# Optimization experiments

Hardware: AMD Instinct MI355X
Metric: run time of the kernel (lower is better)

The kernel has to match this reference:

```python
import jax, jax.numpy as jnp
import numpy as np

N = 65536      # num drones/nodes
E = 262144     # num directed edges
HID = 128      # hidden_dim
HEADS = 8      # gat1 heads
EPS = 1e-5


def _bn(x, g, b):
    # BatchNorm1d in training mode: batch statistics over dim 0 (biased var)
    mu = x.mean(0)
    var = ((x - mu) ** 2).mean(0)
    return (x - mu) * jax.lax.rsqrt(var + EPS) * g + b


def _gat(x, src, dst, W, a_src, a_dst, bias, heads, out_c, n, concat):
    # PyG GATConv math (self-loops already included in src/dst)
    xw = (x @ W).reshape(n, heads, out_c)               # [N,H,C]
    al_s = (xw * a_src).sum(-1)                          # [N,H]
    al_d = (xw * a_dst).sum(-1)                          # [N,H]
    e = jax.nn.leaky_relu(al_s[src] + al_d[dst], 0.2)    # [E',H]
    m = jax.ops.segment_max(e, dst, num_segments=n)      # stable softmax per target
    ex = jnp.exp(e - m[dst])
    den = jax.ops.segment_sum(ex, dst, num_segments=n)
    alpha = ex / den[dst]                                # [E',H]
    out = jax.ops.segment_sum(xw[src] * alpha[:, :, None], dst, num_segments=n)
    out = out.reshape(n, heads * out_c) if concat else out.mean(axis=1)
    return out + bias


def setup_inputs() -> dict:
    key = jax.random.key(0)
    ks = jax.random.split(key, 24)
    s = 0.05
    inp = {
        'node_features': jax.random.normal(ks[0], (N, HID), jnp.float32),
        'relative_poses': jax.random.normal(ks[1], (E, 6), jnp.float32),
        'pe_w1': jax.random.normal(ks[2], (6, 64), jnp.float32) * s,
        'pe_b1': jnp.zeros((64,), jnp.float32),
        'pe_g1': jnp.ones((64,), jnp.float32),
        'pe_be1': jnp.zeros((64,), jnp.float32),
        'pe_w2': jax.random.normal(ks[3], (64, HID), jnp.float32) * s,
        'pe_b2': jnp.zeros((HID,), jnp.float32),
        'pe_g2': jnp.ones((HID,), jnp.float32),
        'pe_be2': jnp.zeros((HID,), jnp.float32),
        'gamma_w': jax.random.normal(ks[4], (HID, HID), jnp.float32) * s,
        'gamma_b': jnp.zeros((HID,), jnp.float32),
        'beta_w': jax.random.normal(ks[5], (HID, HID), jnp.float32) * s,
        'beta_b': jnp.zeros((HID,), jnp.float32),
        'g1_w': jax.random.normal(ks[6], (HID, HEADS * HID), jnp.float32) * s,
        'g1_as': jax.random.normal(ks[7], (HEADS, HID), jnp.float32) * s,
        'g1_ad': jax.random.normal(ks[8], (HEADS, HID), jnp.float32) * s,
        'g1_b': jnp.zeros((HEADS * HID,), jnp.float32),
        'g2_w': jax.random.normal(ks[9], (HEADS * HID, HID), jnp.float32) * s,
        'g2_as': jax.random.normal(ks[10], (1, HID), jnp.float32) * s,
        'g2_ad': jax.random.normal(ks[11], (1, HID), jnp.float32) * s,
        'g2_b': jnp.zeros((HID,), jnp.float32),
        'edge_index': jax.random.randint(ks[12], (2, E), 0, N, jnp.int32),
    }
    return inp


def reference(node_features, relative_poses, pe_w1, pe_b1, pe_g1, pe_be1,
              pe_w2, pe_b2, pe_g2, pe_be2, gamma_w, gamma_b, beta_w, beta_b,
              g1_w, g1_as, g1_ad, g1_b, g2_w, g2_as, g2_ad, g2_b, edge_index):
    src, dst = edge_index[0], edge_index[1]
    # SpatialEncoding: pose MLP with training-mode BN, then FiLM modulation
    h = jax.nn.relu(_bn(relative_poses @ pe_w1 + pe_b1, pe_g1, pe_be1))
    h = jax.nn.relu(_bn(h @ pe_w2 + pe_b2, pe_g2, pe_be2))
    gamma = jax.nn.sigmoid(h @ gamma_w + gamma_b) * 2.0   # [E,HID]
    beta = h @ beta_w + beta_b
    modulated = gamma * node_features[src] + beta          # [E,HID]
    last = jnp.full((N,), -1, jnp.int32).at[dst].max(jnp.arange(E, dtype=jnp.int32))
    enc = jnp.where((last >= 0)[:, None], modulated[jnp.clip(last, 0)], node_features)
    # add self loops (PyG GATConv default)
    loops = jnp.arange(N, dtype=src.dtype)
    src_a = jnp.concatenate([src, loops])
    dst_a = jnp.concatenate([dst, loops])
    x = jax.nn.elu(_gat(enc, src_a, dst_a, g1_w, g1_as, g1_ad, g1_b, HEADS, HID, N, True))
    # dropout is identity in eval mode
    out = _gat(x, src_a, dst_a, g2_w, g2_as, g2_ad, g2_b, 1, HID, N, False)
    return out
```

## Files before the change

### kernel.cpp

```cpp
#include <hip/hip_runtime.h>
#include <hip/hip_bf16.h>
#include <math.h>

#define NN 65536
#define EE 262144

typedef unsigned short u16;
typedef unsigned int u32;
typedef __attribute__((ext_vector_type(8))) short bf16x8;
typedef __attribute__((ext_vector_type(4))) float f32x4;

__device__ __forceinline__ float bfu2f(u16 u){ return __uint_as_float(((u32)u)<<16); }
__device__ __forceinline__ u16 f2bfu(float f){
  u32 x = __float_as_uint(f);
  return (u16)((x + 0x7fffu + ((x>>16)&1u)) >> 16);
}
__device__ __forceinline__ float lrelu(float x){ return x>0.f ? x : 0.2f*x; }
__device__ __forceinline__ float fexp(float x){ return __expf(x); }

__global__ void k_cvtT(const float* __restrict__ B, u16* __restrict__ Bt, int K, int N){
  int idx = blockIdx.x*256+threadIdx.x;
  if (idx < K*N){ int k = idx/N, n = idx - k*N; Bt[n*K+k] = f2bfu(B[idx]); }
}

__global__ void k_cvtn(const float* __restrict__ nf, u16* __restrict__ nfb){
  int i = (blockIdx.x*256+threadIdx.x)*4;
  float4 v = *(const float4*)(nf + i);
  ushort4 o; o.x=f2bfu(v.x); o.y=f2bfu(v.y); o.z=f2bfu(v.z); o.w=f2bfu(v.w);
  *(ushort4*)(nfb + i) = o;
}

__global__ void k_bn1_stats(const float* __restrict__ poses, const float* __restrict__ w1,
                            const float* __restrict__ b1, float* __restrict__ sum1, float* __restrict__ sq1){
  int wave = (blockIdx.x*blockDim.x + threadIdx.x)>>6;
  int c = threadIdx.x & 63;
  float wc[6];
#pragma unroll
  for (int j=0;j<6;++j) wc[j] = w1[j*64+c];
  float bb = b1[c];
  float s=0.f,q=0.f;
  int e0 = wave*(EE/1024);
  for (int e=e0;e<e0+(EE/1024);++e){
    float z = bb;
#pragma unroll
    for (int j=0;j<6;++j) z = fmaf(poses[e*6+j], wc[j], z);
    s += z; q += z*z;
  }
  unsafeAtomicAdd(&sum1[c], s);
  unsafeAtomicAdd(&sq1[c], q);
}

__global__ void k_bn_fin(const float* __restrict__ sum, const float* __restrict__ sq,
                         const float* __restrict__ g, const float* __restrict__ be,
                         const float* __restrict__ bias0,
                         float* __restrict__ a, float* __restrict__ cc, int cols){
  int c = threadIdx.x;
  if (c<cols){
    float mu = sum[c]*(1.f/EE);
    float var = sq[c]*(1.f/EE) - mu*mu;
    float istd = rsqrtf(var + 1e-5f);
    float ac = istd*g[c];
    a[c] = ac;
    float cv = be[c] - mu*ac;
    if (bias0) cv += bias0[c]*ac;
    cc[c] = cv;
  }
}

__global__ void k_red2(const float* __restrict__ psum, const float* __restrict__ psq,
                       float* __restrict__ part2){
  int t = threadIdx.x;
  int b0 = blockIdx.x*128;
  float s = 0.f;
  if (t < 128){
    for (int k=0;k<128;++k) s += psum[(size_t)(b0+k)*128 + t];
  } else {
    int c = t-128;
    for (int k=0;k<128;++k) s += psq[(size_t)(b0+k)*128 + c];
  }
  part2[blockIdx.x*256 + t] = s;
}

__global__ void k_bn_fin2(const float* __restrict__ part2,
                          const float* __restrict__ g, const float* __restrict__ be,
                          const float* __restrict__ bias0,
                          float* __restrict__ a, float* __restrict__ cc){
  int c = threadIdx.x;
  if (c<128){
    float s=0.f,q=0.f;
    for (int k=0;k<32;++k){ s += part2[k*256+c]; q += part2[k*256+128+c]; }
    float mu = s*(1.f/EE);
    float var = q*(1.f/EE) - mu*mu;
    float istd = rsqrtf(var + 1e-5f);
    float ac = istd*g[c];
    a[c] = ac;
    cc[c] = be[c] - mu*ac + bias0[c]*ac;
  }
}

__global__ void k_h1(const float* __restrict__ poses, const float* __restrict__ w1, const float* __restrict__ b1,
                     const float* __restrict__ a1, const float* __restrict__ c1, u16* __restrict__ h1){
  int idx = blockIdx.x*256+threadIdx.x;
  int e = idx>>6, c = idx&63;
  float z = b1[c];
#pragma unroll
  for (int j=0;j<6;++j) z = fmaf(poses[e*6+j], w1[j*64+c], z);
  float h = z*a1[c]+c1[c];
  h1[idx] = f2bfu(h>0.f?h:0.f);
}

template<int EPI>
__launch_bounds__(256)
__global__ void k_mm(const u16* __restrict__ A, const u16* __restrict__ Bt,
                     const u16* __restrict__ Bt2,
                     int K, int lda, int ldbt, int ldc,
                     u16* __restrict__ outb,
                     const float* __restrict__ bias, const float* __restrict__ bias2,
                     float* __restrict__ ssum, float* __restrict__ ssq,
                     const float* __restrict__ gb,
                     const float* __restrict__ bb, const u16* __restrict__ nfselb,
                     const int* __restrict__ lastE){
  const int m0 = blockIdx.x*64, n0 = blockIdx.y*128;
  const int t = threadIdx.x;
  const int lane = t & 63, wv = t>>6;
  const int wr = wv>>1, wc = wv&1;
  __shared__ u16 Als[64*64];
  __shared__ u16 Bls[128*64];
  __shared__ u16 B2ls[EPI==7 ? 128*64 : 8];
  __shared__ float epiS[128][2];
  __shared__ float epiD[128][2];
  f32x4 acc[2][4];
  f32x4 acc2[2][4];
#pragma unroll
  for (int i=0;i<2;++i)
#pragma unroll
    for (int j=0;j<4;++j){ acc[i][j] = (f32x4){0.f,0.f,0.f,0.f}; acc2[i][j] = (f32x4){0.f,0.f,0.f,0.f}; }

  for (int k0=0;k0<K;k0+=64){
    constexpr int NS = (EPI==7) ? 10 : 6;
#pragma unroll
    for (int c=0;c<NS;++c){
      int gc = c*256 + t;
      if (gc < 512){
        int row = gc>>3, ch = gc&7;
        int sw = ((row<<3)|ch) ^ (row&7);
        *(uint4*)(Als + sw*8) = *(const uint4*)(A + (size_t)(m0+row)*lda + k0 + ch*8);
      } else if (gc < 1536){
        int g2 = gc - 512;
        int row = g2>>3, ch = g2&7;
        int sw = ((row<<3)|ch) ^ (row&7);
        *(uint4*)(Bls + sw*8) = *(const uint4*)(Bt + (size_t)(n0+row)*ldbt + k0 + ch*8);
      } else if constexpr (EPI==7){
        int g2 = gc - 1536;
        int row = g2>>3, ch = g2&7;
        int sw = ((row<<3)|ch) ^ (row&7);
        *(uint4*)(B2ls + sw*8) = *(const uint4*)(Bt2 + (size_t)(n0+row)*ldbt + k0 + ch*8);
      }
    }
    __syncthreads();
#pragma unroll
    for (int kk=0;kk<2;++kk){
      bf16x8 af[2], bfr[4];
      int ch = kk*4 + (lane>>4);
#pragma unroll
      for (int i=0;i<2;++i){
        int row = wr*32 + i*16 + (lane&15);
        int sw = ((row<<3)|ch) ^ (row&7);
        af[i] = *(const bf16x8*)(Als + sw*8);
      }
#pragma unroll
      for (int j=0;j<4;++j){
        int rowb = wc*64 + j*16 + (lane&15);
        int swb = ((rowb<<3)|ch) ^ (rowb&7);
        bfr[j] = *(const bf16x8*)(Bls + swb*8);
      }
#pragma unroll
      for (int i=0;i<2;++i)
#pragma unroll
        for (int j=0;j<4;++j)
          acc[i][j] = __builtin_amdgcn_mfma_f32_16x16x32_bf16(af[i], bfr[j], acc[i][j], 0,0,0);
      if constexpr (EPI==7){
        bf16x8 bf2[4];
#pragma unroll
        for (int j=0;j<4;++j){
          int rowb = wc*64 + j*16 + (lane&15);
          int swb = ((rowb<<3)|ch) ^ (rowb&7);
          bf2[j] = *(const bf16x8*)(B2ls + swb*8);
        }
#pragma unroll
        for (int i=0;i<2;++i)
#pragma unroll
          for (int j=0;j<4;++j)
            acc2[i][j] = __builtin_amdgcn_mfma_f32_16x16x32_bf16(af[i], bf2[j], acc2[i][j], 0,0,0);
      }
    }
    __syncthreads();
  }

  int cbase = wc*64 + (lane&15);

  if constexpr (EPI==6){
    float av[4], cv[4];
#pragma unroll
    for (int j=0;j<4;++j){ av[j]=bias[cbase+j*16]; cv[j]=bias2[cbase+j*16]; }
#pragma unroll
    for (int i=0;i<2;++i)
#pragma unroll
      for (int r=0;r<4;++r){
        int row = m0 + wr*32 + i*16 + ((lane>>4)<<2) + r;
#pragma unroll
        for (int j=0;j<4;++j){
          float h = fmaf(acc[i][j][r], av[j], cv[j]);
          outb[(size_t)row*128 + cbase + j*16] = f2bfu(h>0.f?h:0.f);
        }
      }
  } else if constexpr (EPI==2){
    float bv[4];
#pragma unroll
    for (int j=0;j<4;++j) bv[j]=bias[cbase+j*16];
    float s[4]={0,0,0,0}, q[4]={0,0,0,0};
#pragma unroll
    for (int i=0;i<2;++i)
#pragma unroll
      for (int j=0;j<4;++j)
#pragma unroll
        for (int r=0;r<4;++r){ float z = acc[i][j][r]+bv[j]; s[j]+=z; q[j]+=z*z; }
#pragma unroll
    for (int j=0;j<4;++j){
      float ss=s[j], qq=q[j];
      ss += __shfl_xor(ss,16); ss += __shfl_xor(ss,32);
      qq += __shfl_xor(qq,16); qq += __shfl_xor(qq,32);
      if (lane<16){
        epiS[wc*64+j*16+lane][wr] = ss;
        epiD[wc*64+j*16+lane][wr] = qq;
      }
    }
    __syncthreads();
    if (t<128){
      ssum[(size_t)blockIdx.x*128 + t] = epiS[t][0]+epiS[t][1];
      ssq[(size_t)blockIdx.x*128 + t]  = epiD[t][0]+epiD[t][1];
    }
  } else if constexpr (EPI==7){
    float gbv[4], bbv[4];
#pragma unroll
    for (int j=0;j<4;++j){ gbv[j]=gb[cbase+j*16]; bbv[j]=bb[cbase+j*16]; }
#pragma unroll
    for (int i=0;i<2;++i)
#pragma unroll
      for (int r=0;r<4;++r){
        int n = m0 + wr*32 + i*16 + ((lane>>4)<<2) + r;
        int le = lastE[n];
#pragma unroll
        for (int j=0;j<4;++j){
          int c = cbase + j*16;
          float nv = bfu2f(nfselb[(size_t)n*128+c]);
          float res;
          if (le>=0){
            float gp = acc[i][j][r] + gbv[j];
            float gam = 2.f/(1.f+fexp(-gp));
            res = fmaf(gam, nv, acc2[i][j][r] + bbv[j]);
          } else res = nv;
          outb[(size_t)n*128+c] = f2bfu(res);
        }
      }
  }
}

__launch_bounds__(256)
__global__ void k_proj(const u16* __restrict__ aggH, const u16* __restrict__ g1wt,
                       const u16* __restrict__ g2wt, const float* __restrict__ g1b,
                       const float* __restrict__ asv, const float* __restrict__ adv,
                       u16* __restrict__ xw2b, float* __restrict__ als2, float* __restrict__ ald2){
  const int m0 = blockIdx.x*32;
  const int t = threadIdx.x, lane = t&63, wv = t>>6;
  const int wr = wv>>1, wc = wv&1;
  __shared__ u16 ATls[32*128];
  __shared__ u16 Bls[128*64];
  __shared__ float epiS[32][2];
  __shared__ float epiD[32][2];
  u16* Als = ATls;
  u16* Tls = ATls;
  const int cbase = wc*64 + (lane&15);
  f32x4 acc2[4];
#pragma unroll
  for (int j=0;j<4;++j) acc2[j] = (f32x4){0.f,0.f,0.f,0.f};

  for (int hh=0; hh<8; ++hh){
    f32x4 acc1[4];
#pragma unroll
    for (int j=0;j<4;++j) acc1[j] = (f32x4){0.f,0.f,0.f,0.f};
    for (int k0=0;k0<128;k0+=64){
      {
        int row = t>>3, ch = t&7;
        int sw = ((row<<3)|ch) ^ (row&7);
        *(uint4*)(Als + sw*8) = *(const uint4*)(aggH + (size_t)(m0+row)*1024 + hh*128 + k0 + ch*8);
      }
#pragma unroll
      for (int c=0;c<4;++c){
        int g2 = c*256 + t;
        int row = g2>>3, ch = g2&7;
        int sw = ((row<<3)|ch) ^ (row&7);
        *(uint4*)(Bls + sw*8) = *(const uint4*)(g1wt + (size_t)hh*16384 + row*128 + k0 + ch*8);
      }
      __syncthreads();
#pragma unroll
      for (int kk=0;kk<2;++kk){
        bf16x8 af, bfr[4];
        int ch = kk*4 + (lane>>4);
        {
          int row = wr*16 + (lane&15);
          int sw = ((row<<3)|ch) ^ (row&7);
          af = *(const bf16x8*)(Als + sw*8);
        }
#pragma unroll
        for (int j=0;j<4;++j){
          int rowb = wc*64 + j*16 + (lane&15);
          int swb = ((rowb<<3)|ch) ^ (rowb&7);
          bfr[j] = *(const bf16x8*)(Bls + swb*8);
        }
#pragma unroll
        for (int j=0;j<4;++j)
          acc1[j] = __builtin_amdgcn_mfma_f32_16x16x32_bf16(af, bfr[j], acc1[j], 0,0,0);
      }
      __syncthreads();
    }
    {
      float bv[4];
#pragma unroll
      for (int j=0;j<4;++j) bv[j] = g1b[hh*128 + cbase + j*16];
#pragma unroll
      for (int r=0;r<4;++r){
        int m = wr*16 + ((lane>>4)<<2) + r;
#pragma unroll
        for (int j=0;j<4;++j){
          int c = cbase + j*16;
          float v = acc1[j][r] + bv[j];
          v = v>0.f ? v : fexp(v)-1.f;
          int sw = ((m<<4)|(c>>3)) ^ (m&7);
          Tls[sw*8 + (c&7)] = f2bfu(v);
        }
      }
    }
    __syncthreads();
    for (int k0=0;k0<128;k0+=64){
#pragma unroll
      for (int c=0;c<4;++c){
        int g2 = c*256 + t;
        int row = g2>>3, ch = g2&7;
        int sw = ((row<<3)|ch) ^ (row&7);
        *(uint4*)(Bls + sw*8) = *(const uint4*)(g2wt + (size_t)row*1024 + hh*128 + k0 + ch*8);
      }
      __syncthreads();
#pragma unroll
      for (int kk=0;kk<2;++kk){
        bf16x8 af, bfr[4];
        int ch = kk*4 + (lane>>4);
        int chk = (k0>>3) + ch;
        {
          int row = wr*16 + (lane&15);
          int sw = ((row<<4)|chk) ^ (row&7);
          af = *(const bf16x8*)(Tls + sw*8);
        }
#pragma unroll
        for (int j=0;j<4;++j){
          int rowb = wc*64 + j*16 + (lane&15);
          int swb = ((rowb<<3)|ch) ^ (rowb&7);
          bfr[j] = *(const bf16x8*)(Bls + swb*8);
        }
#pragma unroll
        for (int j=0;j<4;++j)
          acc2[j] = __builtin_amdgcn_mfma_f32_16x16x32_bf16(af, bfr[j], acc2[j], 0,0,0);
      }
      __syncthreads();
    }
  }
  float av[4], dv[4];
#pragma unroll
  for (int j=0;j<4;++j){ av[j]=asv[cbase+j*16]; dv[j]=adv[cbase+j*16]; }
#pragma unroll
  for (int r=0;r<4;++r){
    int lr = wr*16 + ((lane>>4)<<2) + r;
    int row = m0 + lr;
    float s=0.f, d=0.f;
#pragma unroll
    for (int j=0;j<4;++j){
      float v = acc2[j][r];
      xw2b[(size_t)row*128 + cbase + j*16] = f2bfu(v);
      s = fmaf(v, av[j], s); d = fmaf(v, dv[j], d);
    }
#pragma unroll
    for (int o=1;o<16;o<<=1){ s += __shfl_xor(s,o); d += __shfl_xor(d,o); }
    if ((lane&15)==0){ epiS[lr][wc]=s; epiD[lr][wc]=d; }
  }
  __syncthreads();
  if (t<32){
    als2[m0+t] = epiS[t][0]+epiS[t][1];
    ald2[m0+t] = epiD[t][0]+epiD[t][1];
  }
}

__global__ void k_lastdeg(const int* __restrict__ dst, int* __restrict__ lastE, int* __restrict__ deg){
  int e = blockIdx.x*256+threadIdx.x;
  int d = dst[e];
  atomicMax(&lastE[d], e);
  atomicAdd(&deg[d], 1);
}
__global__ void k_blocksum(const int* __restrict__ deg, int* __restrict__ bsum){
  __shared__ int s[256];
  int t = threadIdx.x;
  s[t] = deg[blockIdx.x*256+t];
  __syncthreads();
  for (int o=128;o>0;o>>=1){ if (t<o) s[t]+=s[t+o]; __syncthreads(); }
  if (!t) bsum[blockIdx.x]=s[0];
}
__global__ void k_scanb(int* __restrict__ bsum){
  __shared__ int s[256];
  int t=threadIdx.x;
  s[t]=bsum[t]; __syncthreads();
  for (int o=1;o<256;o<<=1){
    int v = s[t];
    if (t>=o) v += s[t-o];
    __syncthreads(); s[t]=v; __syncthreads();
  }
  bsum[t] = t ? s[t-1] : 0;
}
__global__ void k_indptr(const int* __restrict__ deg, const int* __restrict__ bsum, int* __restrict__ indptr){
  __shared__ int s[256];
  int t=threadIdx.x; int g=blockIdx.x*256+t;
  int d = deg[g];
  s[t]=d; __syncthreads();
  for (int o=1;o<256;o<<=1){
    int v = s[t];
    if (t>=o) v += s[t-o];
    __syncthreads(); s[t]=v; __syncthreads();
  }
  indptr[g] = bsum[blockIdx.x] + s[t] - d;
  if (g==NN-1) indptr[NN]=EE;
}
__global__ void k_fill(const int* __restrict__ srcA, const int* __restrict__ dstA,
                       const int* __restrict__ indptr, int* __restrict__ cursor, int* __restrict__ slist){
  int e = blockIdx.x*256+threadIdx.x;
  int d = dstA[e];
  int p = atomicAdd(&cursor[d],1);
  slist[indptr[d]+p] = srcA[e];
}

__global__ void k_gsel(const u16* __restrict__ h1, const u16* __restrict__ nodefb,
                       const int* __restrict__ lastE, const int* __restrict__ srcA,
                       u16* __restrict__ h1sel, u16* __restrict__ nfselb){
  int g = blockIdx.x*256+threadIdx.x;
  int n = g>>4, ch = g&15;
  int le = lastE[n];
  int src = (le>=0) ? srcA[le] : n;
  *(uint4*)(nfselb + (size_t)n*128 + ch*8) = *(const uint4*)(nodefb + (size_t)src*128 + ch*8);
  if (ch < 8){
    uint4 v = make_uint4(0,0,0,0);
    if (le>=0) v = *(const uint4*)(h1 + (size_t)le*64 + ch*8);
    *(uint4*)(h1sel + (size_t)n*64 + ch*8) = v;
  }
}

__global__ void k_vprep(const float* __restrict__ g1w, const float* __restrict__ as_,
                        const float* __restrict__ ad_, u16* __restrict__ vtb){
  int gid = blockIdx.x*256+threadIdx.x;
  if (gid<1024){
    int h = gid>>7, k = gid&127;
    float s=0.f,d=0.f;
    for (int cc=0;cc<128;++cc){
      float wv = g1w[(size_t)k*1024 + h*128+cc];
      s=fmaf(wv,as_[h*128+cc],s); d=fmaf(wv,ad_[h*128+cc],d);
    }
    vtb[h*128+k] = f2bfu(s);
    vtb[(h+8)*128+k] = f2bfu(d);
  }
}

__launch_bounds__(256)
__global__ void k_als1mm(const u16* __restrict__ encb, const u16* __restrict__ vtb,
                         float* __restrict__ als, float* __restrict__ ald){
  int t = threadIdx.x, lane = t&63, wv = t>>6;
  int m0 = blockIdx.x*64 + wv*16;
  f32x4 acc = (f32x4){0.f,0.f,0.f,0.f};
  const u16* arow = encb + (size_t)(m0 + (lane&15))*128;
  const u16* brow = vtb + (lane&15)*128;
  int ko = (lane>>4)*8;
#pragma unroll
  for (int k0=0;k0<128;k0+=32){
    bf16x8 af = *(const bf16x8*)(arow + k0 + ko);
    bf16x8 bf = *(const bf16x8*)(brow + k0 + ko);
    acc = __builtin_amdgcn_mfma_f32_16x16x32_bf16(af, bf, acc, 0,0,0);
  }
  int o = lane&15;
#pragma unroll
  for (int r=0;r<4;++r){
    int row = m0 + ((lane>>4)<<2) + r;
    if (o<8) als[(size_t)row*8+o] = acc[r];
    else     ald[(size_t)row*8+(o-8)] = acc[r];
  }
}

__launch_bounds__(256)
__global__ void k_soft1(const int* __restrict__ slist, const int* __restrict__ indptr,
                        const float* __restrict__ als, const float* __restrict__ ald,
                        float* __restrict__ wcsr, float* __restrict__ den1, float* __restrict__ wself1){
  int t = threadIdx.x;
  int n = blockIdx.x*4 + (t>>6);
  int lane = t&63;
  int ei = lane>>3, h = lane&7;
  int p0 = indptr[n], p1 = indptr[n+1];
  float adh = ald[(size_t)n*8+h];
  float selfsc = lrelu(als[(size_t)n*8+h] + adh);
  float m = selfsc;
  for (int p=p0+ei; p<p1; p+=8){
    int s = slist[p];
    m = fmaxf(m, lrelu(als[(size_t)s*8+h] + adh));
  }
  m = fmaxf(m, __shfl_xor(m,8));
  m = fmaxf(m, __shfl_xor(m,16));
  m = fmaxf(m, __shfl_xor(m,32));
  float ws = fexp(selfsc - m);
  float den = (ei==0) ? ws : 0.f;
  for (int p=p0+ei; p<p1; p+=8){
    int s = slist[p];
    float w = fexp(lrelu(als[(size_t)s*8+h] + adh) - m);
    wcsr[(size_t)p*8+h] = w;
    den += w;
  }
  den += __shfl_xor(den,8);
  den += __shfl_xor(den,16);
  den += __shfl_xor(den,32);
  if (ei==0){
    den1[(size_t)n*8+h] = den;
    wself1[(size_t)n*8+h] = ws;
  }
}

__launch_bounds__(256)
__global__ void k_soft2(const int* __restrict__ slist, const int* __restrict__ indptr,
                        const float* __restrict__ als, const float* __restrict__ ald,
                        float* __restrict__ wcsr, float* __restrict__ den2, float* __restrict__ wself2){
  int t = threadIdx.x;
  int n = blockIdx.x*16 + (t>>4);
  int l = t&15;
  int p0 = indptr[n], p1 = indptr[n+1];
  float adh = ald[n];
  float selfsc = lrelu(als[n] + adh);
  float m = selfsc;
  for (int p=p0+l; p<p1; p+=16)
    m = fmaxf(m, lrelu(als[slist[p]] + adh));
  m = fmaxf(m, __shfl_xor(m,1));
  m = fmaxf(m, __shfl_xor(m,2));
  m = fmaxf(m, __shfl_xor(m,4));
  m = fmaxf(m, __shfl_xor(m,8));
  float ws = fexp(selfsc - m);
  float den = (l==0) ? ws : 0.f;
  for (int p=p0+l; p<p1; p+=16){
    float w = fexp(lrelu(als[slist[p]] + adh) - m);
    wcsr[p] = w;
    den += w;
  }
  den += __shfl_xor(den,1);
  den += __shfl_xor(den,2);
  den += __shfl_xor(den,4);
  den += __shfl_xor(den,8);
  if (l==0){ den2[n] = den; wself2[n] = ws; }
}

__launch_bounds__(256)
__global__ void k_agg1(const u16* __restrict__ encb, const float* __restrict__ wcsr,
                       const float* __restrict__ den1, const float* __restrict__ wself1,
                       const int* __restrict__ slist, const int* __restrict__ indptr,
                       u16* __restrict__ aggH){
  int t = threadIdx.x;
  int n = blockIdx.x*4 + (t>>6);
  int lane = t&63;
  int c0 = lane*2;
  int p0 = indptr[n], p1 = indptr[n+1];
  float a0[8], a1[8];
  {
    ushort2 u = *(const ushort2*)(encb + (size_t)n*128 + c0);
    float x0 = bfu2f(u.x), x1 = bfu2f(u.y);
#pragma unroll
    for (int h=0;h<8;++h){
      float ws = wself1[(size_t)n*8 + h];
      a0[h] = ws*x0; a1[h] = ws*x1;
    }
  }
  for (int p=p0; p<p1; ++p){
    int s = slist[p];
    float4 w0 = *(const float4*)(wcsr + (size_t)p*8);
    float4 w1 = *(const float4*)(wcsr + (size_t)p*8 + 4);
    ushort2 u = *(const ushort2*)(encb + (size_t)s*128 + c0);
    float x0 = bfu2f(u.x), x1 = bfu2f(u.y);
    a0[0]=fmaf(w0.x,x0,a0[0]); a1[0]=fmaf(w0.x,x1,a1[0]);
    a0[1]=fmaf(w0.y,x0,a0[1]); a1[1]=fmaf(w0.y,x1,a1[1]);
    a0[2]=fmaf(w0.z,x0,a0[2]); a1[2]=fmaf(w0.z,x1,a1[2]);
    a0[3]=fmaf(w0.w,x0,a0[3]); a1[3]=fmaf(w0.w,x1,a1[3]);
    a0[4]=fmaf(w1.x,x0,a0[4]); a1[4]=fmaf(w1.x,x1,a1[4]);
    a0[5]=fmaf(w1.y,x0,a0[5]); a1[5]=fmaf(w1.y,x1,a1[5]);
    a0[6]=fmaf(w1.z,x0,a0[6]); a1[6]=fmaf(w1.z,x1,a1[6]);
    a0[7]=fmaf(w1.w,x0,a0[7]); a1[7]=fmaf(w1.w,x1,a1[7]);
  }
#pragma unroll
  for (int h=0;h<8;++h){
    float rr = 1.f/den1[(size_t)n*8 + h];
    u32 pk = (u32)f2bfu(a0[h]*rr) | ((u32)f2bfu(a1[h]*rr)<<16);
    *(u32*)(aggH + (size_t)n*1024 + h*128 + c0) = pk;
  }
}

__launch_bounds__(128)
__global__ void k_gat2(const u16* __restrict__ xw2b, const float* __restrict__ wcsr,
                       const float* __restrict__ den2, const float* __restrict__ wself2,
                       const int* __restrict__ slist, const int* __restrict__ indptr,
                       const float* __restrict__ g2b, float* __restrict__ out){
  int n = blockIdx.x, c = threadIdx.x;
  int p0 = indptr[n], p1 = indptr[n+1];
  float acc = wself2[n]*bfu2f(xw2b[(size_t)n*128+c]);
  int p = p0;
  for (; p+4<=p1; p+=4){
    int s0=slist[p], s1=slist[p+1], s2=slist[p+2], s3=slist[p+3];
    float w0=wcsr[p], w1=wcsr[p+1], w2=wcsr[p+2], w3=wcsr[p+3];
    float x0=bfu2f(xw2b[(size_t)s0*128+c]), x1=bfu2f(xw2b[(size_t)s1*128+c]);
    float x2=bfu2f(xw2b[(size_t)s2*128+c]), x3=bfu2f(xw2b[(size_t)s3*128+c]);
    acc = fmaf(w0,x0,acc); acc = fmaf(w1,x1,acc); acc = fmaf(w2,x2,acc); acc = fmaf(w3,x3,acc);
  }
  for (; p<p1; ++p){
    int s = slist[p];
    acc = fmaf(wcsr[p], bfu2f(xw2b[(size_t)s*128+c]), acc);
  }
  out[(size_t)n*128+c] = acc/den2[n] + g2b[c];
}

extern "C" void kernel_launch(void* const* d_in, const int* in_sizes, int n_in,
                              void* d_out, int out_size, void* d_ws, size_t ws_size,
                              hipStream_t stream){
  const float* nodef  = (const float*)d_in[0];
  const float* poses  = (const float*)d_in[1];
  const float* pe_w1  = (const float*)d_in[2];
  const float* pe_b1  = (const float*)d_in[3];
  const float* pe_g1  = (const float*)d_in[4];
  const float* pe_be1 = (const float*)d_in[5];
  const float* pe_w2  = (const float*)d_in[6];
  const float* pe_b2  = (const float*)d_in[7];
  const float* pe_g2  = (const float*)d_in[8];
  const float* pe_be2 = (const float*)d_in[9];
  const float* gamma_w= (const float*)d_in[10];
  const float* gamma_b= (const float*)d_in[11];
  const float* beta_w = (const float*)d_in[12];
  const float* beta_b = (const float*)d_in[13];
  const float* g1_w   = (const float*)d_in[14];
  const float* g1_as  = (const float*)d_in[15];
  const float* g1_ad  = (const float*)d_in[16];
  const float* g1_b   = (const float*)d_in[17];
  const float* g2_w   = (const float*)d_in[18];
  const float* g2_as  = (const float*)d_in[19];
  const float* g2_ad  = (const float*)d_in[20];
  const float* g2_b   = (const float*)d_in[21];
  const int*   eidx   = (const int*)d_in[22];
  const int* srcA = eidx;
  const int* dstA = eidx + EE;

  char* w = (char*)d_ws;
  const size_t MB = 1048576;
  u16*   aggH  = (u16*)(w + 0);
  u16*   h1    = (u16*)(w + 0);
  u16*   h1sel = (u16*)(w + 32*MB);
  u16*   h2b   = (u16*)(w + 40*MB);
  u16*   nodefb= (u16*)(w + 56*MB);
  u16*   nfselb= (u16*)(w + 72*MB);
  float* psum  = (float*)(w + 88*MB);
  float* psq   = (float*)(w + 90*MB);
  u16*   encb  = (u16*)(w + 128*MB);
  char* sm = w + 144*MB;
  size_t off = 0;
  auto alloc = [&](size_t b)->void*{ void* p = sm+off; off += (b+255)&~(size_t)255; return p; };
  u16* pe_w2t = (u16*)alloc(64*128*2);
  u16* gwt    = (u16*)alloc(128*128*2);
  u16* bwt    = (u16*)alloc(128*128*2);
  u16* g1wt   = (u16*)alloc(1024*128*2);
  u16* g2wt   = (u16*)alloc(128*1024*2);
  u16* vtb    = (u16*)alloc(16*128*2);
  float* part2 = (float*)alloc(32*256*4);
  float* als1  = (float*)alloc((size_t)NN*8*4);
  float* ald1  = (float*)alloc((size_t)NN*8*4);
  float* als2  = (float*)alloc((size_t)NN*4);
  float* ald2  = (float*)alloc((size_t)NN*4);
  float* wself1= (float*)alloc((size_t)NN*8*4);
  float* den1  = (float*)alloc((size_t)NN*8*4);
  float* wcsr1 = (float*)alloc((size_t)EE*8*4);
  float* wself2= (float*)alloc((size_t)NN*4);
  float* den2  = (float*)alloc((size_t)NN*4);
  float* wcsr2 = (float*)alloc((size_t)EE*4);
  u16*  xw2b   = (u16*)alloc((size_t)NN*128*2);
  int* lastE   = (int*)alloc((size_t)NN*4);
  int* deg     = (int*)alloc((size_t)NN*4);
  int* cursor  = (int*)alloc((size_t)NN*4);
  int* indptr  = (int*)alloc((size_t)(NN+1)*4);
  int* slist   = (int*)alloc((size_t)EE*4);
  int* bsum    = (int*)alloc(1024);
  float* stats = (float*)alloc(4096);
  float* sum1 = stats, *sq1 = stats+64;
  float* a1 = stats+384, *c1 = stats+448, *a2 = stats+512, *c2 = stats+640;

  hipMemsetAsync(stats, 0, 384*4, stream);
  hipMemsetAsync(deg, 0, (size_t)NN*4, stream);
  hipMemsetAsync(cursor, 0, (size_t)NN*4, stream);
  hipMemsetAsync(lastE, 0xFF, (size_t)NN*4, stream);

  k_cvtT<<<(64*128+255)/256,256,0,stream>>>(pe_w2, pe_w2t, 64, 128);
  k_cvtT<<<(128*128+255)/256,256,0,stream>>>(gamma_w, gwt, 128, 128);
  k_cvtT<<<(128*128+255)/256,256,0,stream>>>(beta_w, bwt, 128, 128);
  k_cvtT<<<(128*1024+255)/256,256,0,stream>>>(g1_w, g1wt, 128, 1024);
  k_cvtT<<<(1024*128+255)/256,256,0,stream>>>(g2_w, g2wt, 1024, 128);
  k_cvtn<<<NN*128/1024,256,0,stream>>>(nodef, nodefb);
  k_vprep<<<4,256,0,stream>>>(g1_w, g1_as, g1_ad, vtb);

  k_bn1_stats<<<256,256,0,stream>>>(poses, pe_w1, pe_b1, sum1, sq1);
  k_bn_fin<<<1,64,0,stream>>>(sum1, sq1, pe_g1, pe_be1, nullptr, a1, c1, 64);
  k_h1<<<65536,256,0,stream>>>(poses, pe_w1, pe_b1, a1, c1, h1);

  k_mm<2><<<dim3(4096,1),256,0,stream>>>(h1, pe_w2t, nullptr, 64, 64, 64, 0,
      nullptr, pe_b2, nullptr, psum, psq, nullptr, nullptr, nullptr, nullptr);
  k_red2<<<32,256,0,stream>>>(psum, psq, part2);
  k_bn_fin2<<<1,128,0,stream>>>(part2, pe_g2, pe_be2, pe_b2, a2, c2);

  k_lastdeg<<<1024,256,0,stream>>>(dstA, lastE, deg);
  k_blocksum<<<256,256,0,stream>>>(deg, bsum);
  k_scanb<<<1,256,0,stream>>>(bsum);
  k_indptr<<<256,256,0,stream>>>(deg, bsum, indptr);
  k_fill<<<1024,256,0,stream>>>(srcA, dstA, indptr, cursor, slist);

  k_gsel<<<4096,256,0,stream>>>(h1, nodefb, lastE, srcA, h1sel, nfselb);
  k_mm<6><<<dim3(1024,1),256,0,stream>>>(h1sel, pe_w2t, nullptr, 64, 64, 64, 128,
      h2b, a2, c2, nullptr, nullptr, nullptr, nullptr, nullptr, nullptr);

  k_mm<7><<<dim3(1024,1),256,0,stream>>>(h2b, gwt, bwt, 128, 128, 128, 128,
      encb, nullptr, nullptr, nullptr, nullptr, gamma_b, beta_b, nfselb, lastE);

  k_als1mm<<<1024,256,0,stream>>>(encb, vtb, als1, ald1);
  k_soft1<<<NN/4,256,0,stream>>>(slist, indptr, als1, ald1, wcsr1, den1, wself1);

  k_agg1<<<NN/4,256,0,stream>>>(encb, wcsr1, den1, wself1, slist, indptr, aggH);

  k_proj<<<2048,256,0,stream>>>(aggH, g1wt, g2wt, g1_b, g2_as, g2_ad, xw2b, als2, ald2);

  k_soft2<<<NN/16,256,0,stream>>>(slist, indptr, als2, ald2, wcsr2, den2, wself2);
  k_gat2<<<NN,128,0,stream>>>(xw2b, wcsr2, den2, wself2, slist, indptr, g2_b, (float*)d_out);
}
```

Before: 447.4 us.

## Enlarge k_proj row tile to 128 rows with full-K weight staging

```diff
diff --git a/kernel.cpp b/kernel.cpp
--- a/kernel.cpp
+++ b/kernel.cpp
@@ -266,136 +266,145 @@
   }
 }
 
-__launch_bounds__(256)
+__launch_bounds__(256, 2)
 __global__ void k_proj(const u16* __restrict__ aggH, const u16* __restrict__ g1wt,
                        const u16* __restrict__ g2wt, const float* __restrict__ g1b,
                        const float* __restrict__ asv, const float* __restrict__ adv,
                        u16* __restrict__ xw2b, float* __restrict__ als2, float* __restrict__ ald2){
-  const int m0 = blockIdx.x*32;
+  const int m0 = blockIdx.x*128;
   const int t = threadIdx.x, lane = t&63, wv = t>>6;
   const int wr = wv>>1, wc = wv&1;
-  __shared__ u16 ATls[32*128];
-  __shared__ u16 Bls[128*64];
-  __shared__ float epiS[32][2];
-  __shared__ float epiD[32][2];
-  u16* Als = ATls;
-  u16* Tls = ATls;
+  __shared__ u16 ATls[128*128];
+  __shared__ u16 Wls[128*128];
   const int cbase = wc*64 + (lane&15);
-  f32x4 acc2[4];
-#pragma unroll
-  for (int j=0;j<4;++j) acc2[j] = (f32x4){0.f,0.f,0.f,0.f};
+  f32x4 acc2[4][4];
+#pragma unroll
+  for (int i=0;i<4;++i)
+#pragma unroll
+    for (int j=0;j<4;++j) acc2[i][j] = (f32x4){0.f,0.f,0.f,0.f};
 
   for (int hh=0; hh<8; ++hh){
-    f32x4 acc1[4];
-#pragma unroll
-    for (int j=0;j<4;++j) acc1[j] = (f32x4){0.f,0.f,0.f,0.f};
-    for (int k0=0;k0<128;k0+=64){
-      {
-        int row = t>>3, ch = t&7;
-        int sw = ((row<<3)|ch) ^ (row&7);
-        *(uint4*)(Als + sw*8) = *(const uint4*)(aggH + (size_t)(m0+row)*1024 + hh*128 + k0 + ch*8);
-      }
-#pragma unroll
-      for (int c=0;c<4;++c){
-        int g2 = c*256 + t;
-        int row = g2>>3, ch = g2&7;
-        int sw = ((row<<3)|ch) ^ (row&7);
-        *(uint4*)(Bls + sw*8) = *(const uint4*)(g1wt + (size_t)hh*16384 + row*128 + k0 + ch*8);
-      }
-      __syncthreads();
-#pragma unroll
-      for (int kk=0;kk<2;++kk){
-        bf16x8 af, bfr[4];
-        int ch = kk*4 + (lane>>4);
-        {
-          int row = wr*16 + (lane&15);
-          int sw = ((row<<3)|ch) ^ (row&7);
-          af = *(const bf16x8*)(Als + sw*8);
-        }
-#pragma unroll
-        for (int j=0;j<4;++j){
-          int rowb = wc*64 + j*16 + (lane&15);
-          int swb = ((rowb<<3)|ch) ^ (rowb&7);
-          bfr[j] = *(const bf16x8*)(Bls + swb*8);
-        }
+    f32x4 acc1[4][4];
+#pragma unroll
+    for (int i=0;i<4;++i)
+#pragma unroll
+      for (int j=0;j<4;++j) acc1[i][j] = (f32x4){0.f,0.f,0.f,0.f};
+
+#pragma unroll
+    for (int c=0;c<8;++c){
+      int g = c*256 + t;
+      int row = g>>4, ch = g&15;
+      int sw = ((row<<4)|ch) ^ (row&7);
+      *(uint4*)(ATls + sw*8) = *(const uint4*)(aggH + (size_t)(m0+row)*1024 + hh*128 + ch*8);
+    }
+#pragma unroll
+    for (int c=0;c<8;++c){
+      int g = c*256 + t;
+      int row = g>>4, ch = g&15;
+      int sw = ((row<<4)|ch) ^ (row&7);
+      *(uint4*)(Wls + sw*8) = *(const uint4*)(g1wt + (size_t)(hh*128+row)*128 + ch*8);
+    }
+    __syncthreads();
+#pragma unroll
+    for (int kk=0;kk<4;++kk){
+      bf16x8 af[4], bfr[4];
+      int ch = kk*4 + (lane>>4);
+#pragma unroll
+      for (int i=0;i<4;++i){
+        int row = wr*64 + i*16 + (lane&15);
+        int sw = ((row<<4)|ch) ^ (row&7);
+        af[i] = *(const bf16x8*)(ATls + sw*8);
+      }
+#pragma unroll
+      for (int j=0;j<4;++j){
+        int rowb = wc*64 + j*16 + (lane&15);
+        int swb = ((rowb<<4)|ch) ^ (rowb&7);
+        bfr[j] = *(const bf16x8*)(Wls + swb*8);
+      }
+#pragma unroll
+      for (int i=0;i<4;++i)
 #pragma unroll
         for (int j=0;j<4;++j)
-          acc1[j] = __builtin_amdgcn_mfma_f32_16x16x32_bf16(af, bfr[j], acc1[j], 0,0,0);
-      }
-      __syncthreads();
-    }
+          acc1[i][j] = __builtin_amdgcn_mfma_f32_16x16x32_bf16(af[i], bfr[j], acc1[i][j], 0,0,0);
+    }
+    __syncthreads();
     {
       float bv[4];
 #pragma unroll
       for (int j=0;j<4;++j) bv[j] = g1b[hh*128 + cbase + j*16];
 #pragma unroll
-      for (int r=0;r<4;++r){
-        int m = wr*16 + ((lane>>4)<<2) + r;
-#pragma unroll
-        for (int j=0;j<4;++j){
-          int c = cbase + j*16;
-          float v = acc1[j][r] + bv[j];
-          v = v>0.f ? v : fexp(v)-1.f;
-          int sw = ((m<<4)|(c>>3)) ^ (m&7);
-          Tls[sw*8 + (c&7)] = f2bfu(v);
+      for (int i=0;i<4;++i)
+#pragma unroll
+        for (int r=0;r<4;++r){
+          int mrow = wr*64 + i*16 + ((lane>>4)<<2) + r;
+#pragma unroll
+          for (int j=0;j<4;++j){
+            int c = cbase + j*16;
+            float v = acc1[i][j][r] + bv[j];
+            v = v>0.f ? v : fexp(v)-1.f;
+            int sw = ((mrow<<4)|(c>>3)) ^ (mrow&7);
+            ATls[sw*8 + (c&7)] = f2bfu(v);
+          }
         }
-      }
+    }
+#pragma unroll
+    for (int c=0;c<8;++c){
+      int g = c*256 + t;
+      int row = g>>4, ch = g&15;
+      int sw = ((row<<4)|ch) ^ (row&7);
+      *(uint4*)(Wls + sw*8) = *(const uint4*)(g2wt + (size_t)row*1024 + hh*128 + ch*8);
     }
     __syncthreads();
-    for (int k0=0;k0<128;k0+=64){
-#pragma unroll
-      for (int c=0;c<4;++c){
-        int g2 = c*256 + t;
-        int row = g2>>3, ch = g2&7;
-        int sw = ((row<<3)|ch) ^ (row&7);
-        *(uint4*)(Bls + sw*8) = *(const uint4*)(g2wt + (size_t)row*1024 + hh*128 + k0 + ch*8);
-      }
-      __syncthreads();
-#pragma unroll
-      for (int kk=0;kk<2;++kk){
-        bf16x8 af, bfr[4];
-        int ch = kk*4 + (lane>>4);
-        int chk = (k0>>3) + ch;
-        {
-          int row = wr*16 + (lane&15);
-          int sw = ((row<<4)|chk) ^ (row&7);
-          af = *(const bf16x8*)(Tls + sw*8);
-        }
-#pragma unroll
-        for (int j=0;j<4;++j){
-          int rowb = wc*64 + j*16 + (lane&15);
-          int swb = ((rowb<<3)|ch) ^ (rowb&7);
-          bfr[j] = *(const bf16x8*)(Bls + swb*8);
-        }
+#pragma unroll
+    for (int kk=0;kk<4;++kk){
+      bf16x8 af[4], bfr[4];
+      int ch = kk*4 + (lane>>4);
+#pragma unroll
+      for (int i=0;i<4;++i){
+        int row = wr*64 + i*16 + (lane&15);
+        int sw = ((row<<4)|ch) ^ (row&7);
+        af[i] = *(const bf16x8*)(ATls + sw*8);
+      }
+#pragma unroll
+      for (int j=0;j<4;++j){
+        int rowb = wc*64 + j*16 + (lane&15);
+        int swb = ((rowb<<4)|ch) ^ (rowb&7);
+        bfr[j] = *(const bf16x8*)(Wls + swb*8);
+      }
+#pragma unroll
+      for (int i=0;i<4;++i)
 #pragma unroll
         for (int j=0;j<4;++j)
-          acc2[j] = __builtin_amdgcn_mfma_f32_16x16x32_bf16(af, bfr[j], acc2[j], 0,0,0);
-      }
-      __syncthreads();
-    }
-  }
+          acc2[i][j] = __builtin_amdgcn_mfma_f32_16x16x32_bf16(af[i], bfr[j], acc2[i][j], 0,0,0);
+    }
+    __syncthreads();
+  }
+  float* epiS = (float*)ATls;
+  float* epiD = epiS + 256;
   float av[4], dv[4];
 #pragma unroll
   for (int j=0;j<4;++j){ av[j]=asv[cbase+j*16]; dv[j]=adv[cbase+j*16]; }
 #pragma unroll
-  for (int r=0;r<4;++r){
-    int lr = wr*16 + ((lane>>4)<<2) + r;
-    int row = m0 + lr;
-    float s=0.f, d=0.f;
-#pragma unroll
-    for (int j=0;j<4;++j){
-      float v = acc2[j][r];
-      xw2b[(size_t)row*128 + cbase + j*16] = f2bfu(v);
-      s = fmaf(v, av[j], s); d = fmaf(v, dv[j], d);
-    }
-#pragma unroll
-    for (int o=1;o<16;o<<=1){ s += __shfl_xor(s,o); d += __shfl_xor(d,o); }
-    if ((lane&15)==0){ epiS[lr][wc]=s; epiD[lr][wc]=d; }
-  }
+  for (int i=0;i<4;++i)
+#pragma unroll
+    for (int r=0;r<4;++r){
+      int lr = wr*64 + i*16 + ((lane>>4)<<2) + r;
+      int row = m0 + lr;
+      float s=0.f, d=0.f;
+#pragma unroll
+      for (int j=0;j<4;++j){
+        float v = acc2[i][j][r];
+        xw2b[(size_t)row*128 + cbase + j*16] = f2bfu(v);
+        s = fmaf(v, av[j], s); d = fmaf(v, dv[j], d);
+      }
+#pragma unroll
+      for (int o=1;o<16;o<<=1){ s += __shfl_xor(s,o); d += __shfl_xor(d,o); }
+      if ((lane&15)==0){ epiS[lr*2+wc]=s; epiD[lr*2+wc]=d; }
+    }
   __syncthreads();
-  if (t<32){
-    als2[m0+t] = epiS[t][0]+epiS[t][1];
-    ald2[m0+t] = epiD[t][0]+epiD[t][1];
+  if (t<128){
+    als2[m0+t] = epiS[t*2]+epiS[t*2+1];
+    ald2[m0+t] = epiD[t*2]+epiD[t*2+1];
   }
 }
 
@@ -743,7 +752,7 @@
 
   k_agg1<<<NN/4,256,0,stream>>>(encb, wcsr1, den1, wself1, slist, indptr, aggH);
 
-  k_proj<<<2048,256,0,stream>>>(aggH, g1wt, g2wt, g1_b, g2_as, g2_ad, xw2b, als2, ald2);
+  k_proj<<<512,256,0,stream>>>(aggH, g1wt, g2wt, g1_b, g2_as, g2_ad, xw2b, als2, ald2);
 
   k_soft2<<<NN/16,256,0,stream>>>(slist, indptr, als2, ald2, wcsr2, den2, wself2);
   k_gat2<<<NN,128,0,stream>>>(xw2b, wcsr2, den2, wself2, slist, indptr, g2_b, (float*)d_out);
```

After: 591.1 us. 32.1% more time.
